# Optimization experiments

Measured on AMD Instinct MI355X. Metric: run time of the kernel, lower is better.

Reference implementation:

```python
import jax, jax.numpy as jnp
import numpy as np

B, CIN, D, H, W = 2, 64, 64, 64, 64
NUM_CLASSES = 5
STRIDE = 2
NMAX = 32
TOPK = 13
TAL_ALPHA, TAL_BETA = 1.0, 6.0
EPS = 1e-9


def setup_inputs() -> dict:
    key = jax.random.key(0)
    ks = jax.random.split(key, 6)
    features = jax.random.normal(ks[0], (B, CIN, D, H, W), jnp.float32)
    cls_w = jax.random.normal(ks[1], (NUM_CLASSES, CIN, 3, 3, 3), jnp.float32) * 0.02
    cls_b = jnp.zeros((NUM_CLASSES,), jnp.float32)
    off_w = jax.random.normal(ks[2], (3, CIN, 3, 3, 3), jnp.float32) * 0.01
    off_b = jnp.zeros((3,), jnp.float32)
    coords = jax.random.uniform(ks[3], (B, NMAX, 3), jnp.float32, 4.0, float(D * STRIDE) - 4.0)
    cls = jax.random.randint(ks[4], (B, NMAX, 1), 0, NUM_CLASSES).astype(jnp.float32)
    sigma = jax.random.uniform(ks[5], (B, NMAX, 1), jnp.float32, 2.0, 8.0)
    pad = (jnp.arange(NMAX) >= 24)[None, :, None]  # last 8 GT slots are padding
    cls = jnp.where(pad, -100.0, cls)
    labels = jnp.concatenate([coords, cls, sigma], axis=-1)  # B N 5 : x,y,z,class,sigma
    return {"features": features, "cls_w": cls_w, "cls_b": cls_b,
            "off_w": off_w, "off_b": off_b, "labels": labels}


def conv3d(x, w, b):
    y = jax.lax.conv_general_dilated(x, w, (1, 1, 1), 'SAME',
                                     dimension_numbers=('NCDHW', 'OIDHW', 'NCDHW'))
    return y + b[None, :, None, None, None]


def make_anchors():
    g = jnp.stack(jnp.meshgrid(jnp.arange(D), jnp.arange(H), jnp.arange(W), indexing='ij'))
    return (g.astype(jnp.float32) + 0.5) * STRIDE  # (3, D, H, W)


def flatten_bchw(x):
    # B C D H W -> B (D H W) C
    Bsz, C = x.shape[0], x.shape[1]
    return x.transpose(0, 2, 3, 4, 1).reshape(Bsz, -1, C)


def tal_assign(pred_logits, pred_centers, true_labels, true_centers, true_sigmas, valid):
    # pred_logits (B,L,C); pred_centers (B,L,3); true_* (B,N,...); valid (B,N) bool
    Bsz, L, C = pred_logits.shape
    N = true_labels.shape[1]
    d2 = jnp.sum((true_centers[:, :, None, :] - pred_centers[:, None, :, :]) ** 2, -1)  # B N L
    ious = jnp.exp(-d2 / (2.0 * true_sigmas[:, :, None] ** 2))  # keypoint IoU, B N L
    probs = jax.nn.sigmoid(pred_logits).transpose(0, 2, 1)  # B C L
    cls_scores = jnp.take_along_axis(probs, true_labels[:, :, None], axis=1)  # B N L
    align = (cls_scores ** TAL_ALPHA) * (ious ** TAL_BETA)  # alignment metric
    topv, topi = jax.lax.top_k(align, TOPK)
    is_topk = jnp.zeros_like(align).at[
        jnp.arange(Bsz)[:, None, None], jnp.arange(N)[None, :, None], topi
    ].set(jnp.where(topv > EPS, 1.0, 0.0))
    mask_pos = is_topk * valid[:, :, None].astype(align.dtype)  # B N L
    pos_sum = mask_pos.sum(axis=1)  # B L
    # resolve anchors matched to multiple GTs: keep GT with max IoU
    is_max_iou = jax.nn.one_hot(jnp.argmax(ious, axis=1), N, axis=1, dtype=align.dtype)
    mask_pos = jnp.where(pos_sum[:, None, :] > 1, is_max_iou, mask_pos)
    pos_sum = mask_pos.sum(axis=1)
    fg = pos_sum > 0  # B L
    assigned_gt = jnp.argmax(mask_pos, axis=1)  # B L
    assigned_labels = jnp.take_along_axis(true_labels, assigned_gt, axis=1)
    assigned_labels = jnp.where(fg, assigned_labels, C)  # bg_index = C
    assigned_centers = jnp.take_along_axis(true_centers, assigned_gt[:, :, None], axis=1)  # B L 3
    assigned_sigmas = jnp.take_along_axis(true_sigmas, assigned_gt, axis=1)  # B L
    align = align * mask_pos
    max_align = align.max(axis=2, keepdims=True)  # B N 1
    max_iou = (ious * mask_pos).max(axis=2, keepdims=True)
    score = (align * max_iou / (max_align + EPS)).max(axis=1)  # B L
    assigned_scores = jax.nn.one_hot(assigned_labels, C + 1)[..., :C] * score[..., None]  # B L C
    return assigned_labels, assigned_centers, assigned_scores, assigned_sigmas


def detection_loss(logits, offsets, anchors, labels):
    pred_logits = flatten_bchw(logits)               # B L C
    pred_centers = flatten_bchw(anchors + offsets)   # B L 3
    anchor_pts = flatten_bchw(anchors)
    C = pred_logits.shape[-1]
    true_centers = labels[..., :3]
    true_labels_f = labels[..., 3]
    true_sigmas = labels[..., 4]
    valid = true_labels_f != -100.0
    true_labels = jnp.where(valid, true_labels_f, 0.0).astype(jnp.int32)
    assigned = tal_assign(jax.lax.stop_gradient(pred_logits),
                          jax.lax.stop_gradient(pred_centers),
                          true_labels, true_centers, true_sigmas, valid)
    assigned_labels, assigned_centers, assigned_scores, assigned_sigmas = jax.lax.stop_gradient(assigned)
    one_hot_label = jax.nn.one_hot(assigned_labels, C + 1)[..., :C]
    # varifocal loss (alpha=0.75, gamma=2)
    p = jax.nn.sigmoid(pred_logits)
    weight = 0.75 * (p ** 2.0) * (1.0 - one_hot_label) + assigned_scores * one_hot_label
    bce = assigned_scores * jax.nn.softplus(-pred_logits) + (1.0 - assigned_scores) * jax.nn.softplus(pred_logits)
    cls_loss = jnp.sum(weight * bce)
    d = jnp.sum((pred_centers - assigned_centers) ** 2, -1)  # B L
    w = assigned_scores.sum(-1)
    iou = jnp.exp(-d / (2.0 * assigned_sigmas ** 2))
    mask_positive = assigned_labels != C
    reg_loss = jnp.sum(jnp.where(mask_positive, (1.0 - iou) * w, 0.0))
    return (cls_loss + reg_loss) / assigned_scores.sum()


def reference(features, cls_w, cls_b, off_w, off_b, labels):
    logits = conv3d(features, cls_w, cls_b)    # B C D H W
    offsets = conv3d(features, off_w, off_b)   # B 3 D H W
    anchors = jnp.broadcast_to(make_anchors()[None], (features.shape[0], 3, D, H, W))
    loss = detection_loss(logits, offsets, anchors, labels)
    return loss
```

## Files before the change

### kernel.cpp

```cpp
#include <hip/hip_runtime.h>
#include <math.h>

#define NB 2
#define CIN 64
#define DD_ 64
#define HH_ 64
#define WW_ 64
#define NCLS 5
#define LL (DD_*HH_*WW_)
#define NMAXG 32
#define TOPKK 13
#define NSLAB 4
#define ROWS 24
#define BUFSZ (ROWS*1056)

typedef __attribute__((ext_vector_type(16))) float floatx16;

__device__ __forceinline__ float softplusf_(float z){
  return fmaxf(z, 0.f) + log1pf(expf(-fabsf(z)));
}
__device__ __forceinline__ float sigmoidf_(float z){
  return 1.f/(1.f + expf(-z));
}
__device__ __forceinline__ unsigned tofp8_(float x){
  unsigned u = __float_as_uint(x);
  unsigned sign = (u >> 24) & 0x80u;
  unsigned a = u & 0x7FFFFFFFu;
  if (a >= 0x43E00000u) return sign | 0x7Eu;
  if (a < 0x3C800000u){
    float fa = __uint_as_float(a);
    int m = (int)rintf(fa * 512.f);
    return sign | (unsigned)m;
  }
  unsigned bb = a + 0x7FFFFu + ((a >> 20) & 1u);
  unsigned e8 = ((bb >> 23) & 0xFFu) - 120u;
  unsigned m8 = (bb >> 20) & 7u;
  if (e8 > 15u || (e8 == 15u && m8 > 6u)) return sign | 0x7Eu;
  return sign | (e8 << 3) | m8;
}

__global__ __launch_bounds__(256) void transpose_kernel(
    const float* __restrict__ feat, unsigned char* __restrict__ featT,
    const float* __restrict__ cls_w, const float* __restrict__ off_w,
    unsigned char* __restrict__ wA, float* __restrict__ bgz)
{
  const int t = threadIdx.x;
  const int w = t & 63;
  const int hh = t >> 6;
  const int d = blockIdx.x;
  const int h = blockIdx.y*4 + hh;
  const int b = blockIdx.z;
  const float* src = feat + (size_t)b*CIN*LL + (size_t)d*4096 + (size_t)h*64 + w;
  const size_t sp = (size_t)d*4096 + (size_t)h*64 + w;
  #pragma unroll
  for (int cc=0; cc<4; ++cc){
    unsigned q[16];
    #pragma unroll
    for (int j=0;j<16;++j) q[j] = tofp8_(src[(size_t)(cc*16+j)*LL]);
    uint4 p;
    p.x = q[0] | (q[1]<<8) | (q[2]<<16) | (q[3]<<24);
    p.y = q[4] | (q[5]<<8) | (q[6]<<16) | (q[7]<<24);
    p.z = q[8] | (q[9]<<8) | (q[10]<<16) | (q[11]<<24);
    p.w = q[12] | (q[13]<<8) | (q[14]<<16) | (q[15]<<24);
    *(uint4*)(featT + ((size_t)(b*4+cc)*LL + sp)*16) = p;
  }
  if (blockIdx.z == 0 && blockIdx.y == 0 && blockIdx.x < 54){
    if (blockIdx.x == 0 && t < 8) bgz[t] = 0.f;
    int idx = blockIdx.x*256 + t;
    int slice = idx >> 6; int lane = idx & 63;
    int cc = slice & 3; int r = slice >> 2;
    int kw = r % 3; int r2 = r / 3;
    int kh = r2 % 3; int rr = r2 / 3;
    int m = lane & 31, khalf = lane >> 5;
    int outch = m & 7;
    int kd = rr - (m >> 3);
    unsigned q[8];
    #pragma unroll
    for (int i=0;i<8;++i){
      int c = cc*16 + khalf*8 + i;
      float wv = 0.f;
      if (kd >= 0 && kd <= 2){
        if (outch < NCLS) wv = cls_w[(outch*CIN + c)*27 + kd*9 + kh*3 + kw];
        else              wv = off_w[((outch-NCLS)*CIN + c)*27 + kd*9 + kh*3 + kw];
      }
      q[i] = tofp8_(wv);
    }
    uint2 p;
    p.x = q[0] | (q[1]<<8) | (q[2]<<16) | (q[3]<<24);
    p.y = q[4] | (q[5]<<8) | (q[6]<<16) | (q[7]<<24);
    *(uint2*)(wA + (size_t)idx*8) = p;
  }
}

__global__ __launch_bounds__(128, 2) void conv_mfma_kernel(
    const unsigned char* __restrict__ featT,
    const unsigned char* __restrict__ wA,
    const float* __restrict__ cls_b, const float* __restrict__ off_b,
    float* __restrict__ logits_ws,
    float* __restrict__ centers_ws,
    float* __restrict__ bg_sum,
    unsigned* __restrict__ moff_u)
{
  __shared__ uint4 xs4[BUFSZ/16];
  __shared__ float bsum[2];
  unsigned char* xs = (unsigned char*)xs4;

  const int tid = threadIdx.x;
  const int lane = tid & 63, hl = tid >> 6;
  const int col = lane & 31, khalf = lane >> 5;
  const int h0 = blockIdx.x*2, d0 = blockIdx.y*4, b = blockIdx.z;
  const bool edge = (d0==0) || (d0==DD_-4) || (h0==0) || (h0==HH_-2);

  if (tid < 48){
    int row = tid >> 1, slot = tid & 1;
    *(uint4*)(xs + row*1056 + slot*1040) = make_uint4(0,0,0,0);
  }
  if (edge){
    #pragma unroll 1
    for (int row=0; row<ROWS; ++row){
      int d_ = d0-1+(row>>2), h_ = h0-1+(row&3);
      if ((unsigned)d_ < 64u && (unsigned)h_ < 64u) continue;
      if (tid < 64){
        *(uint4*)(xs + row*1056 + (tid+1)*16) = make_uint4(0,0,0,0);
      }
    }
  }

  int soff[12]; int sdst[12]; unsigned svalid = 0;
  #pragma unroll
  for (int it=0; it<12; ++it){
    int row = it*2 + hl;
    int d_ = d0 - 1 + (row>>2), h_ = h0 - 1 + (row&3);
    bool v = !edge || ((unsigned)d_ < 64u && (unsigned)h_ < 64u);
    if (v) svalid |= (1u<<it);
    int dc = v ? d_ : 0, hc = v ? h_ : 0;
    soff[it] = (dc*4096 + hc*64 + lane)*16;
    sdst[it] = row*1056 + 16;
  }

  floatx16 accA0 = (floatx16)(0.f), accA1 = (floatx16)(0.f), accA2 = (floatx16)(0.f);
  floatx16 accB0 = (floatx16)(0.f), accB1 = (floatx16)(0.f), accB2 = (floatx16)(0.f);

  const long* wAv = (const long*)wA;
  const int bpoff = hl*1056 + col*16 + khalf*8;

#define STAGE(ccv) { \
  const unsigned char* plane = featT + (size_t)(b*4+(ccv))*LL*16; \
  _Pragma("unroll") \
  for (int it=0; it<12; ++it){ \
    if (svalid & (1u<<it)){ \
      __builtin_amdgcn_global_load_lds( \
        (const __attribute__((address_space(1))) void*)(plane + soff[it]), \
        (__attribute__((address_space(3))) void*)(xs + sdst[it]), 16, 0, 0); \
    } \
  } }

#define LOADA(dst, ccv, rrv) { \
  _Pragma("unroll") \
  for (int q=0;q<9;++q) dst[q] = wAv[(size_t)(((rrv)*9+q)*4+(ccv))*64 + lane]; }

#define KHW(areg, rrv, khv, aA, aB) \
  if ((unsigned)(h0+hl-1+(khv)) < 64u){ \
    const unsigned char* bp = xs + bpoff + (rrv)*4224 + (khv)*1056; \
    _Pragma("unroll") \
    for (int kw=0;kw<3;++kw){ \
      long a = areg[(khv)*3+kw]; \
      long b0 = *(const long*)(bp + kw*16); \
      aA = __builtin_amdgcn_mfma_f32_32x32x16_fp8_fp8(a, b0, aA, 0,0,0); \
      long b1 = *(const long*)(bp + kw*16 + 512); \
      aB = __builtin_amdgcn_mfma_f32_32x32x16_fp8_fp8(a, b1, aB, 0,0,0); \
    } }

#define COMPR(areg, rrv) \
  if ((unsigned)(d0-1+(rrv)) < 64u){ \
    KHW(areg, rrv, 0, accA0, accB0) \
    KHW(areg, rrv, 1, accA1, accB1) \
    KHW(areg, rrv, 2, accA2, accB2) \
  }

  long aP[9], aQ[9];
  LOADA(aP, 0, 0);

  #pragma unroll 1
  for (int cc=0; cc<4; ++cc){
    if (cc) __syncthreads();
    STAGE(cc);
    __syncthreads();
    LOADA(aQ, cc, 1);             COMPR(aP, 0);
    LOADA(aP, cc, 2);             COMPR(aQ, 1);
    LOADA(aQ, cc, 3);             COMPR(aP, 2);
    LOADA(aP, cc, 4);             COMPR(aQ, 3);
    LOADA(aQ, cc, 5);             COMPR(aP, 4);
    { int nc = (cc+1)&3; LOADA(aP, nc, 0); }  COMPR(aQ, 5);
  }

  floatx16 accA = accA0 + accA1 + accA2;
  floatx16 accB = accB0 + accB1 + accB2;

  float bg = 0.f, om = 0.f;
  const int h = h0 + hl;
  #pragma unroll
  for (int wh=0; wh<2; ++wh){
    const int w = wh*32 + col;
    #pragma unroll
    for (int dq=0; dq<4; ++dq){
      int d = d0 + dq;
      size_t l = (size_t)d*4096 + (size_t)h*64 + w;
      float v0 = wh ? accB[dq*4+0] : accA[dq*4+0];
      float v1 = wh ? accB[dq*4+1] : accA[dq*4+1];
      float v2 = wh ? accB[dq*4+2] : accA[dq*4+2];
      float v3 = wh ? accB[dq*4+3] : accA[dq*4+3];
      if (khalf == 0){
        float z0 = v0 + cls_b[0]; logits_ws[(size_t)(b*NCLS+0)*LL + l] = z0;
        float z1 = v1 + cls_b[1]; logits_ws[(size_t)(b*NCLS+1)*LL + l] = z1;
        float z2 = v2 + cls_b[2]; logits_ws[(size_t)(b*NCLS+2)*LL + l] = z2;
        float z3 = v3 + cls_b[3]; logits_ws[(size_t)(b*NCLS+3)*LL + l] = z3;
        float p;
        p = sigmoidf_(z0); bg += 0.75f*p*p*softplusf_(z0);
        p = sigmoidf_(z1); bg += 0.75f*p*p*softplusf_(z1);
        p = sigmoidf_(z2); bg += 0.75f*p*p*softplusf_(z2);
        p = sigmoidf_(z3); bg += 0.75f*p*p*softplusf_(z3);
      } else {
        float z4 = v0 + cls_b[4]; logits_ws[(size_t)(b*NCLS+4)*LL + l] = z4;
        float p = sigmoidf_(z4); bg += 0.75f*p*p*softplusf_(z4);
        float o0 = v1 + off_b[0];
        float o1 = v2 + off_b[1];
        float o2 = v3 + off_b[2];
        om = fmaxf(om, fmaxf(fabsf(o0), fmaxf(fabsf(o1), fabsf(o2))));
        float4 ctr;
        ctr.x = ((float)d+0.5f)*2.f + o0;
        ctr.y = ((float)h+0.5f)*2.f + o1;
        ctr.z = ((float)w+0.5f)*2.f + o2;
        ctr.w = 0.f;
        *(float4*)(centers_ws + ((size_t)b*LL + l)*4) = ctr;
      }
    }
  }
  #pragma unroll
  for (int off=32;off;off>>=1){
    bg += __shfl_down(bg, off);
    om = fmaxf(om, __shfl_xor(om, off));
  }
  if (lane == 0){
    bsum[hl] = bg;
    atomicMax(moff_u, __float_as_uint(om));
  }
  __syncthreads();
  if (tid == 0)
    atomicAdd(bg_sum, bsum[0]+bsum[1]);
}

__global__ __launch_bounds__(256) void topk_box_kernel(
    const float* __restrict__ logits_ws, const float* __restrict__ centers_ws,
    const float* __restrict__ labels,
    const unsigned* __restrict__ moff_u,
    float* __restrict__ pv, int* __restrict__ pi)
{
  const int bn = blockIdx.x;
  const int slab = blockIdx.y;
  const int b = bn >> 5, n = bn & 31;
  const int tid = threadIdx.x;

  const float* lb = labels + (b*NMAXG + n)*5;
  const float tx = lb[0], ty = lb[1], tz = lb[2];
  const float cf = lb[3];
  const float sg = lb[4];
  const int lab = (cf == -100.f) ? 0 : (int)cf;
  const float m6 = -3.f/(sg*sg);
  const float moff = __uint_as_float(*moff_u);
  const float R = 2.6336f*sg + moff + 0.05f;

  int i0d = (int)ceilf((tx - R - 1.f)*0.5f); if (i0d < 0) i0d = 0;
  int i1d = (int)floorf((tx + R - 1.f)*0.5f); if (i1d > 63) i1d = 63;
  int i0h = (int)ceilf((ty - R - 1.f)*0.5f); if (i0h < 0) i0h = 0;
  int i1h = (int)floorf((ty + R - 1.f)*0.5f); if (i1h > 63) i1h = 63;
  int i0w = (int)ceilf((tz - R - 1.f)*0.5f); if (i0w < 0) i0w = 0;
  int i1w = (int)floorf((tz + R - 1.f)*0.5f); if (i1w > 63) i1w = 63;
  int nd = i1d-i0d+1, nh = i1h-i0h+1, nw = i1w-i0w+1;
  int total = (nd>0 && nh>0 && nw>0) ? nd*nh*nw : 0;
  int lo = (total*slab)/NSLAB, hi = (total*(slab+1))/NSLAB;

  const float* lg = logits_ws + (size_t)(b*NCLS + lab)*LL;
  const float* cb = centers_ws + (size_t)b*LL*4;

  float v[13]; int ix[13];
  #pragma unroll
  for (int j=0;j<13;++j){ v[j]=-1.f; ix[j]=0x7fffffff; }

  for (int idx = lo + tid; idx < hi; idx += 256){
    int r = idx;
    int wi = r % nw; r /= nw;
    int hi2 = r % nh; int di = r / nh;
    int l = (i0d+di)*4096 + (i0h+hi2)*64 + (i0w+wi);
    float4 c4 = *(const float4*)(cb + (size_t)l*4);
    float dx = c4.x-tx, dy = c4.y-ty, dz = c4.z-tz;
    float e = m6*(dx*dx + dy*dy + dz*dz);
    if (e < -20.8f) continue;
    float a = sigmoidf_(lg[l]) * expf(e);
    if (a > v[12]){
      float cv = a; int ci = l;
      #pragma unroll
      for (int j=0;j<13;++j){
        bool take = (cv > v[j]) || (cv == v[j] && ci < ix[j]);
        float nv = take ? cv : v[j];  float ov = take ? v[j] : cv;
        int   ni = take ? ci : ix[j]; int   oi = take ? ix[j] : ci;
        v[j]=nv; ix[j]=ni; cv=ov; ci=oi;
      }
    }
  }

  const int lane = tid & 63, wvi = tid >> 6;
  float mv = -2.f; int mi = 0x7fffffff;
  #pragma unroll 1
  for (int k=0;k<13;++k){
    float bv = v[0]; int bi = ix[0]; int bl = lane;
    #pragma unroll
    for (int off=32; off; off>>=1){
      float ov2 = __shfl_xor(bv, off);
      int oi = __shfl_xor(bi, off);
      int ol = __shfl_xor(bl, off);
      if (ov2 > bv || (ov2 == bv && oi < bi)){ bv=ov2; bi=oi; bl=ol; }
    }
    if (lane == k){ mv = bv; mi = bi; }
    if (lane == bl){
      #pragma unroll
      for (int j=0;j<12;++j){ v[j]=v[j+1]; ix[j]=ix[j+1]; }
      v[12] = -2.f; ix[12] = 0x7fffffff;
    }
  }
  __shared__ float sv2[4*13]; __shared__ int si2[4*13];
  if (lane < 13){ sv2[wvi*13+lane] = mv; si2[wvi*13+lane] = mi; }
  __syncthreads();
  if (wvi == 0){
    float v2 = -2.f; int i2 = 0x7fffffff;
    if (lane < 52){ v2 = sv2[lane]; i2 = si2[lane]; }
    #pragma unroll 1
    for (int k=0;k<13;++k){
      float bv = v2; int bi = i2; int bl = lane;
      #pragma unroll
      for (int off=32; off; off>>=1){
        float ov2 = __shfl_xor(bv, off);
        int oi = __shfl_xor(bi, off);
        int ol = __shfl_xor(bl, off);
        if (ov2 > bv || (ov2 == bv && oi < bi)){ bv=ov2; bi=oi; bl=ol; }
      }
      if (lane == 0){
        pv[(bn*NSLAB+slab)*TOPKK + k] = bv;
        pi[(bn*NSLAB+slab)*TOPKK + k] = bi;
      }
      if (lane == bl) v2 = -2.f;
    }
  }
}

__global__ __launch_bounds__(64) void topk_merge_kernel(
    const float* __restrict__ pv, const int* __restrict__ pi,
    float* __restrict__ tv, int* __restrict__ ti)
{
  const int bn = blockIdx.x;
  const int t = threadIdx.x;
  const int NC = NSLAB*TOPKK;
  float v = -2.f; int ix = 0x7fffffff;
  if (t < NC){ v = pv[bn*NC + t]; ix = pi[bn*NC + t]; }
  #pragma unroll 1
  for (int k=0;k<13;++k){
    float bv = v; int bi = ix; int bl = t;
    #pragma unroll
    for (int off=32; off; off>>=1){
      float ov = __shfl_xor(bv, off);
      int oi = __shfl_xor(bi, off);
      int ol = __shfl_xor(bl, off);
      if (ov > bv || (ov == bv && oi < bi)){ bv=ov; bi=oi; bl=ol; }
    }
    if (t==0){ tv[bn*TOPKK+k]=bv; ti[bn*TOPKK+k]=bi; }
    if (t==bl) v = -2.f;
  }
}

__global__ __launch_bounds__(1024) void finalize_kernel(
    const float* __restrict__ logits_ws, const float* __restrict__ centers_ws,
    const float* __restrict__ labels,
    const float* __restrict__ tv, const int* __restrict__ ti,
    const float* __restrict__ bg_sum, float* __restrict__ out)
{
  const int tid = threadIdx.x;
  __shared__ float gx[64], gy[64], gz[64], gs[64];
  __shared__ int glab[64], gvalid[64];
  __shared__ int hkey[2048], hcnt[2048], hmin[2048];
  __shared__ unsigned maxA[64], maxI[64];
  __shared__ float accD, accC;
  if (tid==0){ accD=0.f; accC=0.f; }
  for (int i=tid;i<2048;i+=1024){ hkey[i]=-1; hcnt[i]=0; hmin[i]=0x7fffffff; }
  if (tid<64){
    const float* lb = labels + tid*5;
    gx[tid]=lb[0]; gy[tid]=lb[1]; gz[tid]=lb[2];
    float cf = lb[3]; gs[tid]=lb[4];
    int val = (cf != -100.f);
    gvalid[tid]=val; glab[tid]= val ? (int)cf : 0;
    maxA[tid]=0u; maxI[tid]=0u;
  }
  __syncthreads();

  const int e = tid;
  bool ok = false; int l = -1; int n = 0; int b = 0;
  if (e < 2*416){
    b = (e >= 416) ? 1 : 0;
    int eb = e - 416*b;
    n = eb/13; int k = eb - 13*n;
    float v = tv[(b*NMAXG+n)*TOPKK + k];
    l = ti[(b*NMAXG+n)*TOPKK + k];
    ok = gvalid[b*32+n] && (v > 1e-9f);
  }
  int slot = -1;
  if (ok){
    unsigned h = (((unsigned)l * 2654435761u) >> 20) & 1023u;
    for (;;){
      int prev = atomicCAS(&hkey[b*1024 + h], -1, l);
      if (prev == -1 || prev == l){ slot = b*1024 + (int)h; break; }
      h = (h+1) & 1023u;
    }
    atomicAdd(&hcnt[slot], 1);
    atomicMin(&hmin[slot], e);
  }
  __syncthreads();

  bool first = ok && (hmin[slot] == e);
  float a=0.f, iou=0.f; int nstar=0;
  if (first){
    float px = centers_ws[((size_t)b*LL + l)*4 + 0];
    float py = centers_ws[((size_t)b*LL + l)*4 + 1];
    float pz = centers_ws[((size_t)b*LL + l)*4 + 2];
    if (hcnt[slot] == 1){
      nstar = n;
    } else {
      float best = -1.f; int bidx = 0;
      #pragma unroll 1
      for (int nn=0;nn<32;++nn){
        float dx=gx[b*32+nn]-px, dy=gy[b*32+nn]-py, dz=gz[b*32+nn]-pz;
        float d2 = dx*dx+dy*dy+dz*dz;
        float io = expf(-d2/(2.f*gs[b*32+nn]*gs[b*32+nn]));
        if (io > best){ best=io; bidx=nn; }
      }
      nstar = bidx;
    }
    int gi = b*32 + nstar;
    float dx=gx[gi]-px, dy=gy[gi]-py, dz=gz[gi]-pz;
    float d2 = dx*dx+dy*dy+dz*dz;
    float sgv = gs[gi];
    iou = expf(-d2/(2.f*sgv*sgv));
    float z = logits_ws[(size_t)(b*NCLS + glab[gi])*LL + l];
    a = sigmoidf_(z) * expf(-3.f*d2/(sgv*sgv));
    atomicMax(&maxA[gi], __float_as_uint(a));
    atomicMax(&maxI[gi], __float_as_uint(iou));
  }
  __syncthreads();

  if (first){
    int gi = b*32 + nstar;
    float mA = __uint_as_float(maxA[gi]);
    float mI = __uint_as_float(maxI[gi]);
    float score = a*mI/(mA + 1e-9f);
    float z = logits_ws[(size_t)(b*NCLS + glab[gi])*LL + l];
    float p = sigmoidf_(z);
    float t2 = log1pf(expf(-fabsf(z)));
    float spz = fmaxf(z,0.f) + t2;
    float spm = fmaxf(-z,0.f) + t2;
    float corr = score*(score*spm + (1.f-score)*spz) - 0.75f*p*p*spz;
    float reg  = (1.f - iou)*score;
    atomicAdd(&accD, score);
    atomicAdd(&accC, corr + reg);
  }
  __syncthreads();
  if (tid==0) out[0] = (bg_sum[0] + accC) / accD;
}

extern "C" void kernel_launch(void* const* d_in, const int* in_sizes, int n_in,
                              void* d_out, int out_size, void* d_ws, size_t ws_size,
                              hipStream_t stream) {
  const float* feat  = (const float*)d_in[0];
  const float* cls_w = (const float*)d_in[1];
  const float* cls_b = (const float*)d_in[2];
  const float* off_w = (const float*)d_in[3];
  const float* off_b = (const float*)d_in[4];
  const float* labels= (const float*)d_in[5];
  float* out = (float*)d_out;

  float* logits_ws  = (float*)d_ws;
  float* centers_ws = logits_ws + (size_t)NB*NCLS*LL;
  float* tv = centers_ws + (size_t)NB*LL*4;
  int*   ti = (int*)(tv + 64*TOPKK);
  float* pv = (float*)(ti + 64*TOPKK);
  int*   pi = (int*)(pv + 64*NSLAB*TOPKK);
  float* bg = (float*)(pi + 64*NSLAB*TOPKK);
  unsigned char* wA = (unsigned char*)(bg + 16);
  unsigned char* featT = wA + 216*64*8;

  transpose_kernel<<<dim3(64,16,2), 256, 0, stream>>>(
      feat, featT, cls_w, off_w, wA, bg);
  conv_mfma_kernel<<<dim3(32,16,2), 128, 0, stream>>>(
      featT, wA, cls_b, off_b, logits_ws, centers_ws, bg, (unsigned*)(bg+1));
  topk_box_kernel<<<dim3(64,NSLAB), 256, 0, stream>>>(
      logits_ws, centers_ws, labels, (const unsigned*)(bg+1), pv, pi);
  topk_merge_kernel<<<64, 64, 0, stream>>>(pv, pi, tv, ti);
  finalize_kernel<<<1, 1024, 0, stream>>>(
      logits_ws, centers_ws, labels, tv, ti, bg, out);
}
```

Measured before the change: 171.1 us.

## Give each wave a private LDS slab and drop block barriers in conv

The shared 24-row LDS tile used by both waves is replaced with a private 18-row region per wave. Each wave stages its own halo rows and waits only on its own vector-memory counter, so the two __syncthreads per channel chunk go away. The intent is to let the two waves run independently and overlap loads with MFMA work. The cost is duplicated halo rows, which means more global-to-LDS traffic and a larger LDS footprint per block.

```diff
diff --git a/kernel.cpp b/kernel.cpp
--- a/kernel.cpp
+++ b/kernel.cpp
@@ -11,8 +11,7 @@
 #define NMAXG 32
 #define TOPKK 13
 #define NSLAB 4
-#define ROWS 24
-#define BUFSZ (ROWS*1056)
+#define WREG 19008
 
 typedef __attribute__((ext_vector_type(16))) float floatx16;
 
@@ -101,7 +100,7 @@
     float* __restrict__ bg_sum,
     unsigned* __restrict__ moff_u)
 {
-  __shared__ uint4 xs4[BUFSZ/16];
+  __shared__ uint4 xs4[2*WREG/16];
   __shared__ float bsum[2];
   unsigned char* xs = (unsigned char*)xs4;
 
@@ -111,43 +110,42 @@
   const int h0 = blockIdx.x*2, d0 = blockIdx.y*4, b = blockIdx.z;
   const bool edge = (d0==0) || (d0==DD_-4) || (h0==0) || (h0==HH_-2);
 
-  if (tid < 48){
-    int row = tid >> 1, slot = tid & 1;
-    *(uint4*)(xs + row*1056 + slot*1040) = make_uint4(0,0,0,0);
+  unsigned char* reg_ = xs + hl*WREG;
+
+  if (lane < 36){
+    int row = lane >> 1, slot = lane & 1;
+    *(uint4*)(reg_ + row*1056 + slot*1040) = make_uint4(0,0,0,0);
   }
   if (edge){
     #pragma unroll 1
-    for (int row=0; row<ROWS; ++row){
-      int d_ = d0-1+(row>>2), h_ = h0-1+(row&3);
+    for (int row=0; row<18; ++row){
+      int d_ = d0-1+row/3, h_ = h0+hl-1+row%3;
       if ((unsigned)d_ < 64u && (unsigned)h_ < 64u) continue;
-      if (tid < 64){
-        *(uint4*)(xs + row*1056 + (tid+1)*16) = make_uint4(0,0,0,0);
-      }
-    }
-  }
-
-  int soff[12]; int sdst[12]; unsigned svalid = 0;
+      *(uint4*)(reg_ + row*1056 + (lane+1)*16) = make_uint4(0,0,0,0);
+    }
+  }
+
+  int soff[18]; int sdst[18]; unsigned svalid = 0;
   #pragma unroll
-  for (int it=0; it<12; ++it){
-    int row = it*2 + hl;
-    int d_ = d0 - 1 + (row>>2), h_ = h0 - 1 + (row&3);
+  for (int it=0; it<18; ++it){
+    int d_ = d0 - 1 + it/3, h_ = h0 + hl - 1 + it%3;
     bool v = !edge || ((unsigned)d_ < 64u && (unsigned)h_ < 64u);
     if (v) svalid |= (1u<<it);
     int dc = v ? d_ : 0, hc = v ? h_ : 0;
     soff[it] = (dc*4096 + hc*64 + lane)*16;
-    sdst[it] = row*1056 + 16;
+    sdst[it] = hl*WREG + it*1056 + 16;
   }
 
   floatx16 accA0 = (floatx16)(0.f), accA1 = (floatx16)(0.f), accA2 = (floatx16)(0.f);
   floatx16 accB0 = (floatx16)(0.f), accB1 = (floatx16)(0.f), accB2 = (floatx16)(0.f);
 
   const long* wAv = (const long*)wA;
-  const int bpoff = hl*1056 + col*16 + khalf*8;
+  const int bpoff = hl*WREG + col*16 + khalf*8;
 
 #define STAGE(ccv) { \
   const unsigned char* plane = featT + (size_t)(b*4+(ccv))*LL*16; \
   _Pragma("unroll") \
-  for (int it=0; it<12; ++it){ \
+  for (int it=0; it<18; ++it){ \
     if (svalid & (1u<<it)){ \
       __builtin_amdgcn_global_load_lds( \
         (const __attribute__((address_space(1))) void*)(plane + soff[it]), \
@@ -161,7 +159,7 @@
 
 #define KHW(areg, rrv, khv, aA, aB) \
   if ((unsigned)(h0+hl-1+(khv)) < 64u){ \
-    const unsigned char* bp = xs + bpoff + (rrv)*4224 + (khv)*1056; \
+    const unsigned char* bp = xs + bpoff + (rrv)*3168 + (khv)*1056; \
     _Pragma("unroll") \
     for (int kw=0;kw<3;++kw){ \
       long a = areg[(khv)*3+kw]; \
@@ -183,9 +181,8 @@
 
   #pragma unroll 1
   for (int cc=0; cc<4; ++cc){
-    if (cc) __syncthreads();
     STAGE(cc);
-    __syncthreads();
+    asm volatile("s_waitcnt vmcnt(0)" ::: "memory");
     LOADA(aQ, cc, 1);             COMPR(aP, 0);
     LOADA(aP, cc, 2);             COMPR(aQ, 1);
     LOADA(aQ, cc, 3);             COMPR(aP, 2);
```

After: 175.9 us. 2.8% more time.
